# Optimization experiments

Measured on AMD Instinct MI355X. Metric: run time of the kernel, lower is better.

The kernel has to match this reference:

```python
import jax, jax.numpy as jnp
import numpy as np

HIDDEN = 2048
N_EXPERTS = 8
TOP_K = 2
MOE_INTER = 1408
NORM_TOPK = False  # config.norm_topk_prob


def setup_inputs() -> dict:
    key = jax.random.key(0)
    k0, k1, k2, k3, k4 = jax.random.split(key, 5)
    hidden_states = jax.random.normal(k0, (2, 2048, HIDDEN), dtype=jnp.float32)
    # router gate: nn.Linear(hidden, num_experts, bias=False) -> store as [H, E]
    gate_w = jax.random.normal(k1, (HIDDEN, N_EXPERTS), dtype=jnp.float32) * 0.02
    # per-expert MLP weights, stacked over experts (Linear is x @ W.T, stored pre-transposed)
    w_gate = jax.random.normal(k2, (N_EXPERTS, HIDDEN, MOE_INTER), dtype=jnp.float32) * 0.02
    w_up = jax.random.normal(k3, (N_EXPERTS, HIDDEN, MOE_INTER), dtype=jnp.float32) * 0.02
    w_down = jax.random.normal(k4, (N_EXPERTS, MOE_INTER, HIDDEN), dtype=jnp.float32) * 0.02
    return {"hidden_states": hidden_states, "gate_w": gate_w,
            "w_gate": w_gate, "w_up": w_up, "w_down": w_down}


def reference(hidden_states, gate_w, w_gate, w_up, w_down):
    B, S, H = hidden_states.shape
    x = hidden_states.reshape(-1, H)                      # [T, H]
    T = x.shape[0]
    router_logits = x @ gate_w                            # [T, E]
    probs = jax.nn.softmax(router_logits.astype(jnp.float32), axis=-1)
    routing_weights, selected = jax.lax.top_k(probs, TOP_K)  # [T, K], [T, K]
    if NORM_TOPK:
        routing_weights = routing_weights / routing_weights.sum(-1, keepdims=True)
    routing_weights = routing_weights.astype(x.dtype)
    # dense combine weights [T, E]: scatter top-k weights to expert slots
    combine = jnp.zeros((T, N_EXPERTS), dtype=x.dtype)
    combine = combine.at[jnp.arange(T)[:, None], selected].add(routing_weights)
    # run all experts densely (reference form of gather-MLP-scatter)
    g = jnp.einsum('th,ehf->tef', x, w_gate)              # [T, E, F]
    u = jnp.einsum('th,ehf->tef', x, w_up)
    h = jax.nn.silu(g) * u
    y = jnp.einsum('tef,efh->teh', h, w_down)             # [T, E, H]
    out = jnp.einsum('te,teh->th', combine, y)            # [T, H]
    return out
```

## Files before the change

### kernel.cpp

```cpp
#include <hip/hip_runtime.h>
#include <hip/hip_bf16.h>

#define HID  2048
#define NEXP 8
#define FINT 1408
#define TM   256
#define GU_NPAN 88
#define DN_NPAN 64

typedef __bf16 bf16_t;
typedef __bf16 bf16x8 __attribute__((ext_vector_type(8)));
typedef float  f32x4  __attribute__((ext_vector_type(4)));

#define AS1 __attribute__((address_space(1)))
#define AS3 __attribute__((address_space(3)))

__device__ __forceinline__ void gll16(const void* g, void* l) {
    __builtin_amdgcn_global_load_lds((const AS1 void*)g, (AS3 void*)l, 16, 0, 0);
}

#define VM4() asm volatile("s_waitcnt vmcnt(4)" ::: "memory")
#define VM2() asm volatile("s_waitcnt vmcnt(2)" ::: "memory")
#define VM0() asm volatile("s_waitcnt vmcnt(0)" ::: "memory")
#define LGKM0()  asm volatile("s_waitcnt lgkmcnt(0)" ::: "memory")
#define SB0() __builtin_amdgcn_sched_barrier(0)

__global__ __launch_bounds__(64) void router_kernel(
    const float* __restrict__ x, const float* __restrict__ gw,
    int* __restrict__ cnt, int* __restrict__ topk_id, float* __restrict__ topk_w,
    bf16_t* __restrict__ xb, int T)
{
    int t = blockIdx.x;
    if (t >= T) return;
    int lane = threadIdx.x;
    float acc[NEXP];
#pragma unroll
    for (int e = 0; e < NEXP; ++e) acc[e] = 0.f;
    const float* xr = x + (size_t)t * HID;
    bf16_t* xo = xb + (size_t)t * HID;
    for (int i0 = lane * 4; i0 < HID; i0 += 256) {
        float4 xv = *(const float4*)(xr + i0);
        bf16_t b4[4] = {(bf16_t)xv.x, (bf16_t)xv.y, (bf16_t)xv.z, (bf16_t)xv.w};
        *(uint2*)(xo + i0) = *(uint2*)b4;
        float xs[4] = {xv.x, xv.y, xv.z, xv.w};
#pragma unroll
        for (int u = 0; u < 4; ++u) {
            const float4* g4 = (const float4*)(gw + (size_t)(i0 + u) * NEXP);
            float4 a = g4[0], b = g4[1];
            acc[0] += xs[u] * a.x; acc[1] += xs[u] * a.y; acc[2] += xs[u] * a.z; acc[3] += xs[u] * a.w;
            acc[4] += xs[u] * b.x; acc[5] += xs[u] * b.y; acc[6] += xs[u] * b.z; acc[7] += xs[u] * b.w;
        }
    }
#pragma unroll
    for (int d = 1; d < 64; d <<= 1) {
#pragma unroll
        for (int e = 0; e < NEXP; ++e) acc[e] += __shfl_xor(acc[e], d, 64);
    }
    float mx = acc[0];
#pragma unroll
    for (int e = 1; e < NEXP; ++e) mx = fmaxf(mx, acc[e]);
    float p[NEXP]; float s = 0.f;
#pragma unroll
    for (int e = 0; e < NEXP; ++e) { p[e] = expf(acc[e] - mx); s += p[e]; }
    float inv = 1.f / s;
    int i1 = 0;
#pragma unroll
    for (int e = 1; e < NEXP; ++e) if (acc[e] > acc[i1]) i1 = e;
    int i2 = (i1 == 0) ? 1 : 0;
#pragma unroll
    for (int e = 0; e < NEXP; ++e) if (e != i1 && acc[e] > acc[i2]) i2 = e;
    if (lane == 0) {
        topk_id[t * 2 + 0] = i1; topk_id[t * 2 + 1] = i2;
        topk_w[t * 2 + 0] = p[i1] * inv; topk_w[t * 2 + 1] = p[i2] * inv;
        atomicAdd(&cnt[i1], 1); atomicAdd(&cnt[i2], 1);
    }
}

__global__ void offsets_kernel(const int* __restrict__ cnt, int* __restrict__ offs,
                               int* __restrict__ gbase, int* __restrict__ gcount,
                               int* __restrict__ dbase, int* __restrict__ dcount,
                               int* __restrict__ gu, int* __restrict__ dn)
{
    __shared__ int gc[8], dc[8];
    int tid = threadIdx.x;
    if (tid == 0) {
        int s = 0;
        for (int e = 0; e < NEXP; ++e) { offs[e] = s; s += cnt[e]; }
        offs[NEXP] = s;
    }
    if (tid < 8) {
        int c = 0;
        for (int p = tid; p < GU_NPAN; p += 8) { int e = p / 11; c += (cnt[e] + TM - 1) / TM; }
        gc[tid] = c;
    } else if (tid < 16) {
        int x = tid - 8, c = 0;
        for (int p = x; p < DN_NPAN; p += 8) { int e = p >> 3; c += (cnt[e] + TM - 1) / TM; }
        dc[x] = c;
    }
    __syncthreads();
    if (tid < 8) {
        int base = 0;
        for (int i = 0; i < tid; ++i) base += gc[i];
        gbase[tid] = base; gcount[tid] = gc[tid];
        int k = base;
        for (int p = tid; p < GU_NPAN; p += 8) {
            int e = p / 11, fp = p - e * 11;
            int nt = (cnt[e] + TM - 1) / TM;
            for (int t = 0; t < nt; ++t) gu[k++] = (e << 10) | (fp << 6) | t;
        }
    } else if (tid < 16) {
        int x = tid - 8;
        int base = 0;
        for (int i = 0; i < x; ++i) base += dc[i];
        dbase[x] = base; dcount[x] = dc[x];
        int k = base;
        for (int p = x; p < DN_NPAN; p += 8) {
            int e = p >> 3, hp = p & 7;
            int nt = (cnt[e] + TM - 1) / TM;
            for (int t = 0; t < nt; ++t) dn[k++] = (e << 10) | (hp << 6) | t;
        }
    }
}

__global__ void scatter_kernel(
    const int* __restrict__ topk_id, const int* __restrict__ offs, int* __restrict__ fill,
    int* __restrict__ tok, int* __restrict__ slot_of, int T)
{
    int t = blockIdx.x * blockDim.x + threadIdx.x;
    if (t >= T) return;
#pragma unroll
    for (int k = 0; k < 2; ++k) {
        int e = topk_id[t * 2 + k];
        int pos = atomicAdd(&fill[e], 1);
        int slot = offs[e] + pos;
        tok[slot] = t;
        slot_of[t * 2 + k] = slot;
    }
}

__global__ __launch_bounds__(256) void cvt3_kernel(
    const float* __restrict__ wg, const float* __restrict__ wu, const float* __restrict__ wd,
    bf16_t* __restrict__ wgb, bf16_t* __restrict__ wub, bf16_t* __restrict__ wdb)
{
    const int per = NEXP * (HID / 64) * (FINT / 64);
    int b = blockIdx.x;
    const float* in; bf16_t* outb; int R, C;
    if (b < per)            { in = wg; outb = wgb; R = HID;  C = FINT; }
    else if (b < 2 * per)   { b -= per; in = wu; outb = wub; R = HID;  C = FINT; }
    else                    { b -= 2 * per; in = wd; outb = wdb; R = FINT; C = HID; }

    int tilesC = C >> 6;
    int perE = (R >> 6) * tilesC;
    int e = b / perE;
    int rem = b - e * perE;
    int tr = rem / tilesC, tc = rem - tr * tilesC;
    const float* src = in + (size_t)e * R * C + (size_t)(tr * 64) * C + tc * 64;
    bf16_t* dst = outb + (size_t)e * R * C + (size_t)(tc * 64) * R + tr * 64;

    __shared__ float tile[64][65];
    int tid = threadIdx.x;
    int rr = tid >> 4;
    int cc = (tid & 15) * 4;
#pragma unroll
    for (int i = 0; i < 4; ++i) {
        float4 v = *(const float4*)(src + (size_t)(rr + i * 16) * C + cc);
        tile[rr + i * 16][cc + 0] = v.x; tile[rr + i * 16][cc + 1] = v.y;
        tile[rr + i * 16][cc + 2] = v.z; tile[rr + i * 16][cc + 3] = v.w;
    }
    __syncthreads();
    int oc = tid >> 2;
    int og = (tid & 3) * 16;
    bf16_t* dp = dst + (size_t)oc * R + og;
    bf16x8 o0, o1;
#pragma unroll
    for (int j = 0; j < 8; ++j) { o0[j] = (bf16_t)tile[og + j][oc]; o1[j] = (bf16_t)tile[og + 8 + j][oc]; }
    *(bf16x8*)dp = o0;
    *(bf16x8*)(dp + 8) = o1;
}


__global__ __launch_bounds__(512, 1) void gateup4_kernel(
    const bf16_t* __restrict__ xb, const bf16_t* __restrict__ wgb, const bf16_t* __restrict__ wub,
    const int* __restrict__ offs, const int* __restrict__ tok,
    const int* __restrict__ gbase, const int* __restrict__ gcount, const int* __restrict__ gu,
    bf16_t* __restrict__ h_buf)
{
    __shared__ bf16_t smem[65536];
    const int tid = threadIdx.x;
    const int lane = tid & 63, w = tid >> 6;
    const int wr = w >> 2, wc = w & 3;
    const int lr = lane & 15, lg = lane >> 4;
    const int sw7 = lr & 7;
    const int ksrc = ((lane & 7) ^ ((lane >> 3) & 7)) * 8;
    int iS[2];
#pragma unroll
    for (int j = 0; j < 2; ++j) iS[j] = w * 16 + j * 8 + (lane >> 3);
    const int dA[2] = { (w * 128 + 0) * 8, (w * 128 + 64) * 8 };

    const int xcd = blockIdx.x & 7, slot = blockIdx.x >> 3;
    const int icnt = gcount[xcd], ib = gbase[xcd];

    for (int ii = slot; ii < icnt; ii += 32) {
        const int it = gu[ib + ii];
        const int e = it >> 10, fp = (it >> 6) & 15, tr = it & 63;
        const int seg0 = offs[e];
        const int rbase = tr * TM;
        const int nvalid = min(offs[e + 1] - seg0 - rbase, TM);
        const int row0 = seg0 + rbase;
        const int f0 = fp * 128;

        const bf16_t* aSrc[2][2];
        const bf16_t* bSrc[2];
#pragma unroll
        for (int j = 0; j < 2; ++j) {
            int rA0 = ((iS[j] >> 6) << 7) + (iS[j] & 63);
#pragma unroll
            for (int mh = 0; mh < 2; ++mh) {
                int rA = rA0 + mh * 64;
                int tk = tok[row0 + min(rA, nvalid - 1)];
                aSrc[j][mh] = xb + (size_t)tk * HID + ksrc;
            }
            int rB = ((iS[j] >> 5) << 6) + (iS[j] & 31);
            const bf16_t* W = (rB < 128) ? wgb : wub;
            bSrc[j] = W + ((size_t)e * FINT + f0 + (rB & 127)) * HID + ksrc;
        }

        f32x4 acc[8][4];
#pragma unroll
        for (int mf = 0; mf < 8; ++mf)
#pragma unroll
            for (int nf = 0; nf < 4; ++nf) acc[mf][nf] = (f32x4){0.f, 0.f, 0.f, 0.f};

        auto SG_A = [&](int bb, int kt, int mh) {
#pragma unroll
            for (int j = 0; j < 2; ++j)
                gll16(aSrc[j][mh] + kt * 64, &smem[bb * 16384 + mh * 8192 + dA[j]]);
        };
        auto SG_B = [&](int bb, int kt, int nh) {
#pragma unroll
            for (int j = 0; j < 2; ++j)
                gll16(bSrc[j] + (size_t)nh * 32 * HID + kt * 64, &smem[32768 + bb * 16384 + nh * 8192 + dA[j]]);
        };

#define GU_READ_MFMA(BB, MH, NH)                                                              \
        {                                                                                     \
            bf16x8 afr[4][2], bfr[2][2];                                                      \
            _Pragma("unroll")                                                                 \
            for (int m = 0; m < 4; ++m)                                                       \
                _Pragma("unroll")                                                             \
                for (int ks = 0; ks < 2; ++ks)                                                \
                    afr[m][ks] = *(const bf16x8*)&smem[(BB) * 16384 + (MH) * 8192 +           \
                        (wr * 64 + m * 16 + lr) * 64 + (((ks * 4 + lg) ^ sw7)) * 8];          \
            _Pragma("unroll")                                                                 \
            for (int n = 0; n < 2; ++n)                                                       \
                _Pragma("unroll")                                                             \
                for (int ks = 0; ks < 2; ++ks)                                                \
                    bfr[n][ks] = *(const bf16x8*)&smem[32768 + (BB) * 16384 + (NH) * 8192 +   \
                        (wc * 32 + n * 16 + lr) * 64 + (((ks * 4 + lg) ^ sw7)) * 8];          \
            LGKM0(); SB0();                                                                   \
            __builtin_amdgcn_s_setprio(1);                                                    \
            _Pragma("unroll")                                                                 \
            for (int m = 0; m < 4; ++m)                                                       \
                _Pragma("unroll")                                                             \
                for (int n = 0; n < 2; ++n)                                                   \
                    _Pragma("unroll")                                                         \
                    for (int ks = 0; ks < 2; ++ks)                                            \
                        acc[(MH) * 4 + m][(NH) * 2 + n] = __builtin_amdgcn_mfma_f32_16x16x32_bf16( \
                            afr[m][ks], bfr[n][ks], acc[(MH) * 4 + m][(NH) * 2 + n], 0, 0, 0); \
            __builtin_amdgcn_s_setprio(0);                                                    \
        }

        const int NK = HID / 64;
        SG_B(0, 0, 0); SG_A(0, 0, 0); SG_A(0, 0, 1); SG_B(0, 0, 1);
        for (int kt = 0; kt < NK; ++kt) {
            const int bb = kt & 1, nb = bb ^ 1;
            const bool nl = (kt + 1 < NK);
            SB0(); LGKM0(); VM4(); __builtin_amdgcn_s_barrier(); SB0();
            if (nl) SG_B(nb, kt + 1, 0);
            GU_READ_MFMA(bb, 0, 0);
            SB0(); LGKM0(); if (nl) { VM4(); } else { VM2(); } __builtin_amdgcn_s_barrier(); SB0();
            if (nl) SG_A(nb, kt + 1, 0);
            GU_READ_MFMA(bb, 1, 0);
            SB0(); LGKM0(); if (nl) { VM4(); } else { VM0(); } __builtin_amdgcn_s_barrier(); SB0();
            if (nl) SG_A(nb, kt + 1, 1);
            GU_READ_MFMA(bb, 0, 1);
            if (nl) SG_B(nb, kt + 1, 1);
            GU_READ_MFMA(bb, 1, 1);
        }
        __syncthreads();

        if (wc >= 2) {
#pragma unroll
            for (int mf = 0; mf < 8; ++mf)
#pragma unroll
                for (int nf = 0; nf < 4; ++nf)
#pragma unroll
                    for (int rr = 0; rr < 4; ++rr) {
                        int row = wr * 128 + mf * 16 + lg * 4 + rr;
                        int col = (wc - 2) * 64 + nf * 16 + lr;
                        smem[row * 128 + col] = (bf16_t)acc[mf][nf][rr];
                    }
        }
        __syncthreads();
        if (wc < 2) {
#pragma unroll
            for (int mf = 0; mf < 8; ++mf)
#pragma unroll
                for (int nf = 0; nf < 4; ++nf)
#pragma unroll
                    for (int rr = 0; rr < 4; ++rr) {
                        int row = wr * 128 + mf * 16 + lg * 4 + rr;
                        int col = wc * 64 + nf * 16 + lr;
                        float g = acc[mf][nf][rr];
                        float u = (float)smem[row * 128 + col];
                        float h = (g / (1.f + __expf(-g))) * u;
                        if (row < nvalid)
                            h_buf[(size_t)(row0 + row) * FINT + f0 + col] = (bf16_t)h;
                    }
        }
        __syncthreads();
    }
#undef GU_READ_MFMA
}

__global__ __launch_bounds__(512, 1) void down4_kernel(
    const bf16_t* __restrict__ h_buf, const bf16_t* __restrict__ wdb,
    const int* __restrict__ offs,
    const int* __restrict__ dbase, const int* __restrict__ dcount, const int* __restrict__ dn,
    bf16_t* __restrict__ y_buf)
{
    __shared__ bf16_t smem[65536];
    const int tid = threadIdx.x;
    const int lane = tid & 63, w = tid >> 6;
    const int wr = w >> 2, wc = w & 3;
    const int lr = lane & 15, lg = lane >> 4;
    const int sw7 = lr & 7;
    const int ksrc = ((lane & 7) ^ ((lane >> 3) & 7)) * 8;
    int iS[2];
#pragma unroll
    for (int j = 0; j < 2; ++j) iS[j] = w * 16 + j * 8 + (lane >> 3);
    const int dA[2] = { (w * 128 + 0) * 8, (w * 128 + 64) * 8 };

    const int xcd = blockIdx.x & 7, slot = blockIdx.x >> 3;
    const int icnt = dcount[xcd], ib = dbase[xcd];

    for (int ii = slot; ii < icnt; ii += 32) {
        const int it = dn[ib + ii];
        const int e = it >> 10, hp = (it >> 6) & 15, tr = it & 63;
        const int seg0 = offs[e];
        const int rbase = tr * TM;
        const int nvalid = min(offs[e + 1] - seg0 - rbase, TM);
        const int row0 = seg0 + rbase;
        const int h0 = hp * 256;

        const bf16_t* aSrc[2][2];
        const bf16_t* bSrc[2];
#pragma unroll
        for (int j = 0; j < 2; ++j) {
            int rA0 = ((iS[j] >> 6) << 7) + (iS[j] & 63);
#pragma unroll
            for (int mh = 0; mh < 2; ++mh)
                aSrc[j][mh] = h_buf + (size_t)(row0 + rA0 + mh * 64) * FINT + ksrc;
            int rB = ((iS[j] >> 5) << 6) + (iS[j] & 31);
            bSrc[j] = wdb + ((size_t)e * HID + h0 + rB) * FINT + ksrc;
        }

        f32x4 acc[8][4];
#pragma unroll
        for (int mf = 0; mf < 8; ++mf)
#pragma unroll
            for (int nf = 0; nf < 4; ++nf) acc[mf][nf] = (f32x4){0.f, 0.f, 0.f, 0.f};

        auto SG_A = [&](int bb, int kt, int mh) {
#pragma unroll
            for (int j = 0; j < 2; ++j)
                gll16(aSrc[j][mh] + kt * 64, &smem[bb * 16384 + mh * 8192 + dA[j]]);
        };
        auto SG_B = [&](int bb, int kt, int nh) {
#pragma unroll
            for (int j = 0; j < 2; ++j)
                gll16(bSrc[j] + (size_t)nh * 32 * FINT + kt * 64, &smem[32768 + bb * 16384 + nh * 8192 + dA[j]]);
        };

#define DN_READ_MFMA(BB, MH, NH)                                                              \
        {                                                                                     \
            bf16x8 afr[4][2], bfr[2][2];                                                      \
            _Pragma("unroll")                                                                 \
            for (int m = 0; m < 4; ++m)                                                       \
                _Pragma("unroll")                                                             \
                for (int ks = 0; ks < 2; ++ks)                                                \
                    afr[m][ks] = *(const bf16x8*)&smem[(BB) * 16384 + (MH) * 8192 +           \
                        (wr * 64 + m * 16 + lr) * 64 + (((ks * 4 + lg) ^ sw7)) * 8];          \
            _Pragma("unroll")                                                                 \
            for (int n = 0; n < 2; ++n)                                                       \
                _Pragma("unroll")                                                             \
                for (int ks = 0; ks < 2; ++ks)                                                \
                    bfr[n][ks] = *(const bf16x8*)&smem[32768 + (BB) * 16384 + (NH) * 8192 +   \
                        (wc * 32 + n * 16 + lr) * 64 + (((ks * 4 + lg) ^ sw7)) * 8];          \
            LGKM0(); SB0();                                                                   \
            __builtin_amdgcn_s_setprio(1);                                                    \
            _Pragma("unroll")                                                                 \
            for (int m = 0; m < 4; ++m)                                                       \
                _Pragma("unroll")                                                             \
                for (int n = 0; n < 2; ++n)                                                   \
                    _Pragma("unroll")                                                         \
                    for (int ks = 0; ks < 2; ++ks)                                            \
                        acc[(MH) * 4 + m][(NH) * 2 + n] = __builtin_amdgcn_mfma_f32_16x16x32_bf16( \
                            afr[m][ks], bfr[n][ks], acc[(MH) * 4 + m][(NH) * 2 + n], 0, 0, 0); \
            __builtin_amdgcn_s_setprio(0);                                                    \
        }

        const int NK = FINT / 64;
        SG_B(0, 0, 0); SG_A(0, 0, 0); SG_A(0, 0, 1); SG_B(0, 0, 1);
        for (int kt = 0; kt < NK; ++kt) {
            const int bb = kt & 1, nb = bb ^ 1;
            const bool nl = (kt + 1 < NK);
            SB0(); LGKM0(); VM4(); __builtin_amdgcn_s_barrier(); SB0();
            if (nl) SG_B(nb, kt + 1, 0);
            DN_READ_MFMA(bb, 0, 0);
            SB0(); LGKM0(); if (nl) { VM4(); } else { VM2(); } __builtin_amdgcn_s_barrier(); SB0();
            if (nl) SG_A(nb, kt + 1, 0);
            DN_READ_MFMA(bb, 1, 0);
            SB0(); LGKM0(); if (nl) { VM4(); } else { VM0(); } __builtin_amdgcn_s_barrier(); SB0();
            if (nl) SG_A(nb, kt + 1, 1);
            DN_READ_MFMA(bb, 0, 1);
            if (nl) SG_B(nb, kt + 1, 1);
            DN_READ_MFMA(bb, 1, 1);
        }

#pragma unroll
        for (int mf = 0; mf < 8; ++mf)
#pragma unroll
            for (int nf = 0; nf < 4; ++nf)
#pragma unroll
                for (int rr = 0; rr < 4; ++rr) {
                    int row = wr * 128 + mf * 16 + lg * 4 + rr;
                    int col = wc * 64 + nf * 16 + lr;
                    if (row < nvalid)
                        y_buf[(size_t)(row0 + row) * HID + h0 + col] = (bf16_t)acc[mf][nf][rr];
                }
        __syncthreads();
    }
#undef DN_READ_MFMA
}

__global__ __launch_bounds__(256) void combine_kernel(
    const bf16_t* __restrict__ y, const int* __restrict__ slot_of,
    const float* __restrict__ topk_w, float* __restrict__ out, int T)
{
    int t = blockIdx.x;
    int tid = threadIdx.x;
    int s0 = slot_of[t * 2], s1 = slot_of[t * 2 + 1];
    float w0 = topk_w[t * 2], w1 = topk_w[t * 2 + 1];
    const bf16x8* y0 = (const bf16x8*)(y + (size_t)s0 * HID);
    const bf16x8* y1 = (const bf16x8*)(y + (size_t)s1 * HID);
    bf16x8 v0 = y0[tid], v1 = y1[tid];
    float* op = out + (size_t)t * HID + tid * 8;
#pragma unroll
    for (int j = 0; j < 8; ++j)
        op[j] = w0 * (float)v0[j] + w1 * (float)v1[j];
}

extern "C" void kernel_launch(void* const* d_in, const int* in_sizes, int n_in,
                              void* d_out, int out_size, void* d_ws, size_t ws_size,
                              hipStream_t stream)
{
    const float* x  = (const float*)d_in[0];
    const float* gw = (const float*)d_in[1];
    const float* wg = (const float*)d_in[2];
    const float* wu = (const float*)d_in[3];
    const float* wd = (const float*)d_in[4];
    float* out = (float*)d_out;
    int T = in_sizes[0] / HID;
    int S2 = 2 * T;

    char* base = (char*)d_ws;
    int* cnt     = (int*)base;
    int* fill    = cnt + 8;
    int* offs    = cnt + 16;
    int* gbase   = cnt + 32;
    int* gcount  = cnt + 40;
    int* dbase   = cnt + 48;
    int* dcount  = cnt + 56;
    int* gu      = cnt + 64;
    int* dnl     = cnt + 576;
    int* topk_id = cnt + 960;
    float* topk_w = (float*)(topk_id + S2);
    int* tok     = (int*)(topk_w + S2);
    int* slot_of = tok + S2 + 256;
    size_t small_end = (size_t)((char*)(slot_of + S2) - base);
    size_t cur = (small_end + 255) & ~(size_t)255;
    auto take = [&](size_t bytes) -> size_t {
        size_t o = cur; cur += bytes; cur = (cur + 255) & ~(size_t)255; return o;
    };
    size_t wbytes = (size_t)NEXP * HID * FINT * 2;
    size_t o_xb  = take((size_t)T * HID * 2);
    size_t o_wgb = take(wbytes);
    size_t o_wub = take(wbytes);
    size_t o_wdb = take(wbytes);
    size_t o_h   = take((size_t)(S2 + 256) * FINT * 2);
    size_t o_y   = take((size_t)(S2 + 256) * HID * 2);
    (void)ws_size;

    bf16_t* xb    = (bf16_t*)(base + o_xb);
    bf16_t* wgb   = (bf16_t*)(base + o_wgb);
    bf16_t* wub   = (bf16_t*)(base + o_wub);
    bf16_t* wdb   = (bf16_t*)(base + o_wdb);
    bf16_t* h_buf = (bf16_t*)(base + o_h);
    bf16_t* y_buf = (bf16_t*)(base + o_y);

    hipMemsetAsync(base, 0, 64, stream);

    router_kernel<<<T, 64, 0, stream>>>(x, gw, cnt, topk_id, topk_w, xb, T);
    offsets_kernel<<<1, 64, 0, stream>>>(cnt, offs, gbase, gcount, dbase, dcount, gu, dnl);
    scatter_kernel<<<(T + 255) / 256, 256, 0, stream>>>(topk_id, offs, fill, tok, slot_of, T);

    int gridW = 3 * NEXP * (HID / 64) * (FINT / 64);
    cvt3_kernel<<<gridW, 256, 0, stream>>>(wg, wu, wd, wgb, wub, wdb);

    gateup4_kernel<<<256, 512, 0, stream>>>(xb, wgb, wub, offs, tok, gbase, gcount, gu, h_buf);
    down4_kernel<<<256, 512, 0, stream>>>(h_buf, wdb, offs, dbase, dcount, dnl, y_buf);
    combine_kernel<<<T, 256, 0, stream>>>(y_buf, slot_of, topk_w, out, T);
}
```

Measured before the change: 479.6 us.

## Reorder GEMM main loop into 8-phase schedule reusing A/B fragments across MFMA blocks

Restructures the gate-up and down GEMM main loops so LDS fragment reads, global-to-LDS prefetches and MFMA blocks follow an explicit 8-phase barrier schedule. A fragments are read once per half and reused across two N halves, cutting redundant LDS reads. Prefetches for the next tile are issued right after each read phase. This adds more barriers per k-step and reorders the issue of the prefetched halves, which may add sync overhead.

```diff
diff --git a/kernel.cpp b/kernel.cpp
--- a/kernel.cpp
+++ b/kernel.cpp
@@ -24,6 +24,7 @@
 #define VM0() asm volatile("s_waitcnt vmcnt(0)" ::: "memory")
 #define LGKM0()  asm volatile("s_waitcnt lgkmcnt(0)" ::: "memory")
 #define SB0() __builtin_amdgcn_sched_barrier(0)
+#define BAR() __builtin_amdgcn_s_barrier()
 
 __global__ __launch_bounds__(64) void router_kernel(
     const float* __restrict__ x, const float* __restrict__ gw,
@@ -179,6 +180,35 @@
 }
 
 
+#define RD_A(MH)                                                                           \
+    { _Pragma("unroll")                                                                    \
+      for (int m = 0; m < 4; ++m)                                                          \
+        _Pragma("unroll")                                                                  \
+        for (int ks = 0; ks < 2; ++ks)                                                     \
+          afr[m][ks] = *(const bf16x8*)&smem[bb * 16384 + (MH) * 8192 +                    \
+              (wr * 64 + m * 16 + lr) * 64 + (((ks * 4 + lg) ^ sw7)) * 8]; }
+
+#define RD_B(NH)                                                                           \
+    { _Pragma("unroll")                                                                    \
+      for (int n = 0; n < 2; ++n)                                                          \
+        _Pragma("unroll")                                                                  \
+        for (int ks = 0; ks < 2; ++ks)                                                     \
+          bfr[n][ks] = *(const bf16x8*)&smem[32768 + bb * 16384 + (NH) * 8192 +            \
+              (wc * 32 + n * 16 + lr) * 64 + (((ks * 4 + lg) ^ sw7)) * 8]; }
+
+#define DO_MFMA(MH, NH)                                                                    \
+    { LGKM0(); SB0();                                                                      \
+      __builtin_amdgcn_s_setprio(1);                                                       \
+      _Pragma("unroll")                                                                    \
+      for (int m = 0; m < 4; ++m)                                                          \
+        _Pragma("unroll")                                                                  \
+        for (int n = 0; n < 2; ++n)                                                        \
+          _Pragma("unroll")                                                                \
+          for (int ks = 0; ks < 2; ++ks)                                                   \
+            acc[(MH) * 4 + m][(NH) * 2 + n] = __builtin_amdgcn_mfma_f32_16x16x32_bf16(     \
+                afr[m][ks], bfr[n][ks], acc[(MH) * 4 + m][(NH) * 2 + n], 0, 0, 0);         \
+      __builtin_amdgcn_s_setprio(0); }
+
 __global__ __launch_bounds__(512, 1) void gateup4_kernel(
     const bf16_t* __restrict__ xb, const bf16_t* __restrict__ wgb, const bf16_t* __restrict__ wub,
     const int* __restrict__ offs, const int* __restrict__ tok,
@@ -231,61 +261,44 @@
 #pragma unroll
             for (int nf = 0; nf < 4; ++nf) acc[mf][nf] = (f32x4){0.f, 0.f, 0.f, 0.f};
 
-        auto SG_A = [&](int bb, int kt, int mh) {
+        auto SG_A = [&](int bbuf, int kt, int mh) {
 #pragma unroll
             for (int j = 0; j < 2; ++j)
-                gll16(aSrc[j][mh] + kt * 64, &smem[bb * 16384 + mh * 8192 + dA[j]]);
+                gll16(aSrc[j][mh] + kt * 64, &smem[bbuf * 16384 + mh * 8192 + dA[j]]);
         };
-        auto SG_B = [&](int bb, int kt, int nh) {
+        auto SG_B = [&](int bbuf, int kt, int nh) {
 #pragma unroll
             for (int j = 0; j < 2; ++j)
-                gll16(bSrc[j] + (size_t)nh * 32 * HID + kt * 64, &smem[32768 + bb * 16384 + nh * 8192 + dA[j]]);
+                gll16(bSrc[j] + (size_t)nh * 32 * HID + kt * 64, &smem[32768 + bbuf * 16384 + nh * 8192 + dA[j]]);
         };
 
-#define GU_READ_MFMA(BB, MH, NH)                                                              \
-        {                                                                                     \
-            bf16x8 afr[4][2], bfr[2][2];                                                      \
-            _Pragma("unroll")                                                                 \
-            for (int m = 0; m < 4; ++m)                                                       \
-                _Pragma("unroll")                                                             \
-                for (int ks = 0; ks < 2; ++ks)                                                \
-                    afr[m][ks] = *(const bf16x8*)&smem[(BB) * 16384 + (MH) * 8192 +           \
-                        (wr * 64 + m * 16 + lr) * 64 + (((ks * 4 + lg) ^ sw7)) * 8];          \
-            _Pragma("unroll")                                                                 \
-            for (int n = 0; n < 2; ++n)                                                       \
-                _Pragma("unroll")                                                             \
-                for (int ks = 0; ks < 2; ++ks)                                                \
-                    bfr[n][ks] = *(const bf16x8*)&smem[32768 + (BB) * 16384 + (NH) * 8192 +   \
-                        (wc * 32 + n * 16 + lr) * 64 + (((ks * 4 + lg) ^ sw7)) * 8];          \
-            LGKM0(); SB0();                                                                   \
-            __builtin_amdgcn_s_setprio(1);                                                    \
-            _Pragma("unroll")                                                                 \
-            for (int m = 0; m < 4; ++m)                                                       \
-                _Pragma("unroll")                                                             \
-                for (int n = 0; n < 2; ++n)                                                   \
-                    _Pragma("unroll")                                                         \
-                    for (int ks = 0; ks < 2; ++ks)                                            \
-                        acc[(MH) * 4 + m][(NH) * 2 + n] = __builtin_amdgcn_mfma_f32_16x16x32_bf16( \
-                            afr[m][ks], bfr[n][ks], acc[(MH) * 4 + m][(NH) * 2 + n], 0, 0, 0); \
-            __builtin_amdgcn_s_setprio(0);                                                    \
-        }
-
         const int NK = HID / 64;
-        SG_B(0, 0, 0); SG_A(0, 0, 0); SG_A(0, 0, 1); SG_B(0, 0, 1);
+        SG_A(0, 0, 0); SG_B(0, 0, 0); SG_B(0, 0, 1); SG_A(0, 0, 1);
+        VM4(); BAR();
+        bf16x8 afr[4][2], bfr[2][2];
         for (int kt = 0; kt < NK; ++kt) {
             const int bb = kt & 1, nb = bb ^ 1;
             const bool nl = (kt + 1 < NK);
-            SB0(); LGKM0(); VM4(); __builtin_amdgcn_s_barrier(); SB0();
+            RD_A(0); RD_B(0);
+            if (nl) SG_A(nb, kt + 1, 0);
+            SB0(); BAR();
+            DO_MFMA(0, 0);
+            SB0(); if (nl) { VM4(); } else { VM2(); } BAR();
+            RD_B(1);
             if (nl) SG_B(nb, kt + 1, 0);
-            GU_READ_MFMA(bb, 0, 0);
-            SB0(); LGKM0(); if (nl) { VM4(); } else { VM2(); } __builtin_amdgcn_s_barrier(); SB0();
-            if (nl) SG_A(nb, kt + 1, 0);
-            GU_READ_MFMA(bb, 1, 0);
-            SB0(); LGKM0(); if (nl) { VM4(); } else { VM0(); } __builtin_amdgcn_s_barrier(); SB0();
+            SB0(); BAR();
+            DO_MFMA(0, 1);
+            SB0(); if (nl) { VM4(); } else { VM0(); } BAR();
+            RD_A(1); RD_B(0);
+            if (nl) SG_B(nb, kt + 1, 1);
+            SB0(); BAR();
+            DO_MFMA(1, 0);
+            SB0(); BAR();
+            RD_B(1);
             if (nl) SG_A(nb, kt + 1, 1);
-            GU_READ_MFMA(bb, 0, 1);
-            if (nl) SG_B(nb, kt + 1, 1);
-            GU_READ_MFMA(bb, 1, 1);
+            SB0(); BAR();
+            DO_MFMA(1, 1);
+            SB0(); if (nl) { VM4(); } BAR();
         }
         __syncthreads();
 
@@ -320,7 +333,6 @@
         }
         __syncthreads();
     }
-#undef GU_READ_MFMA
 }
 
 __global__ __launch_bounds__(512, 1) void down4_kernel(
@@ -371,61 +383,44 @@
 #pragma unroll
             for (int nf = 0; nf < 4; ++nf) acc[mf][nf] = (f32x4){0.f, 0.f, 0.f, 0.f};
 
-        auto SG_A = [&](int bb, int kt, int mh) {
+        auto SG_A = [&](int bbuf, int kt, int mh) {
 #pragma unroll
             for (int j = 0; j < 2; ++j)
-                gll16(aSrc[j][mh] + kt * 64, &smem[bb * 16384 + mh * 8192 + dA[j]]);
+                gll16(aSrc[j][mh] + kt * 64, &smem[bbuf * 16384 + mh * 8192 + dA[j]]);
         };
-        auto SG_B = [&](int bb, int kt, int nh) {
+        auto SG_B = [&](int bbuf, int kt, int nh) {
 #pragma unroll
             for (int j = 0; j < 2; ++j)
-                gll16(bSrc[j] + (size_t)nh * 32 * FINT + kt * 64, &smem[32768 + bb * 16384 + nh * 8192 + dA[j]]);
+                gll16(bSrc[j] + (size_t)nh * 32 * FINT + kt * 64, &smem[32768 + bbuf * 16384 + nh * 8192 + dA[j]]);
         };
 
-#define DN_READ_MFMA(BB, MH, NH)                                                              \
-        {                                                                                     \
-            bf16x8 afr[4][2], bfr[2][2];                                                      \
-            _Pragma("unroll")                                                                 \
-            for (int m = 0; m < 4; ++m)                                                       \
-                _Pragma("unroll")                                                             \
-                for (int ks = 0; ks < 2; ++ks)                                                \
-                    afr[m][ks] = *(const bf16x8*)&smem[(BB) * 16384 + (MH) * 8192 +           \
-                        (wr * 64 + m * 16 + lr) * 64 + (((ks * 4 + lg) ^ sw7)) * 8];          \
-            _Pragma("unroll")                                                                 \
-            for (int n = 0; n < 2; ++n)                                                       \
-                _Pragma("unroll")                                                             \
-                for (int ks = 0; ks < 2; ++ks)                                                \
-                    bfr[n][ks] = *(const bf16x8*)&smem[32768 + (BB) * 16384 + (NH) * 8192 +   \
-                        (wc * 32 + n * 16 + lr) * 64 + (((ks * 4 + lg) ^ sw7)) * 8];          \
-            LGKM0(); SB0();                                                                   \
-            __builtin_amdgcn_s_setprio(1);                                                    \
-            _Pragma("unroll")                                                                 \
-            for (int m = 0; m < 4; ++m)                                                       \
-                _Pragma("unroll")                                                             \
-                for (int n = 0; n < 2; ++n)                                                   \
-                    _Pragma("unroll")                                                         \
-                    for (int ks = 0; ks < 2; ++ks)                                            \
-                        acc[(MH) * 4 + m][(NH) * 2 + n] = __builtin_amdgcn_mfma_f32_16x16x32_bf16( \
-                            afr[m][ks], bfr[n][ks], acc[(MH) * 4 + m][(NH) * 2 + n], 0, 0, 0); \
-            __builtin_amdgcn_s_setprio(0);                                                    \
-        }
-
         const int NK = FINT / 64;
-        SG_B(0, 0, 0); SG_A(0, 0, 0); SG_A(0, 0, 1); SG_B(0, 0, 1);
+        SG_A(0, 0, 0); SG_B(0, 0, 0); SG_B(0, 0, 1); SG_A(0, 0, 1);
+        VM4(); BAR();
+        bf16x8 afr[4][2], bfr[2][2];
         for (int kt = 0; kt < NK; ++kt) {
             const int bb = kt & 1, nb = bb ^ 1;
             const bool nl = (kt + 1 < NK);
-            SB0(); LGKM0(); VM4(); __builtin_amdgcn_s_barrier(); SB0();
+            RD_A(0); RD_B(0);
+            if (nl) SG_A(nb, kt + 1, 0);
+            SB0(); BAR();
+            DO_MFMA(0, 0);
+            SB0(); if (nl) { VM4(); } else { VM2(); } BAR();
+            RD_B(1);
             if (nl) SG_B(nb, kt + 1, 0);
-            DN_READ_MFMA(bb, 0, 0);
-            SB0(); LGKM0(); if (nl) { VM4(); } else { VM2(); } __builtin_amdgcn_s_barrier(); SB0();
-            if (nl) SG_A(nb, kt + 1, 0);
-            DN_READ_MFMA(bb, 1, 0);
-            SB0(); LGKM0(); if (nl) { VM4(); } else { VM0(); } __builtin_amdgcn_s_barrier(); SB0();
+            SB0(); BAR();
+            DO_MFMA(0, 1);
+            SB0(); if (nl) { VM4(); } else { VM0(); } BAR();
+            RD_A(1); RD_B(0);
+            if (nl) SG_B(nb, kt + 1, 1);
+            SB0(); BAR();
+            DO_MFMA(1, 0);
+            SB0(); BAR();
+            RD_B(1);
             if (nl) SG_A(nb, kt + 1, 1);
-            DN_READ_MFMA(bb, 0, 1);
-            if (nl) SG_B(nb, kt + 1, 1);
-            DN_READ_MFMA(bb, 1, 1);
+            SB0(); BAR();
+            DO_MFMA(1, 1);
+            SB0(); if (nl) { VM4(); } BAR();
         }
 
 #pragma unroll
@@ -441,7 +436,6 @@
                 }
         __syncthreads();
     }
-#undef DN_READ_MFMA
 }
 
 __global__ __launch_bounds__(256) void combine_kernel(
```

Result: no change. 487.5 us (+1.7%).
